# Optimization experiments

Hardware: AMD Instinct MI355X
Metric: run time of the kernel (lower is better)

Reference implementation:

```python
import jax, jax.numpy as jnp
import numpy as np

EMBED = 512
HEADS = 8
SCALE = 4
B, N = 2, 2048
DH = EMBED // HEADS
EPS = 1e-5


def _mha(q_in, k_in, v_in, wq, bq, wk, bk, wv, bv, wo, bo, causal):
    Bq, Nq, _ = q_in.shape
    Nk = k_in.shape[1]
    Q = (q_in @ wq + bq).reshape(Bq, Nq, HEADS, DH)
    K = (k_in @ wk + bk).reshape(Bq, Nk, HEADS, DH)
    V = (v_in @ wv + bv).reshape(Bq, Nk, HEADS, DH)
    # scores: [B, H, Nq, Nk]
    scores = jnp.einsum('bqhd,bkhd->bhqk', Q, K) / np.sqrt(DH).astype(np.float32)
    if causal:
        mask = jnp.triu(jnp.full((Nq, Nq), -jnp.inf, dtype=scores.dtype), k=1)
        scores = scores + mask[None, None]
    attn = jax.nn.softmax(scores, axis=-1)
    out = jnp.einsum('bhqk,bkhd->bqhd', attn, V).reshape(Bq, Nq, EMBED)
    return out @ wo + bo


def _ln(x, g, b):
    mu = jnp.mean(x, axis=-1, keepdims=True)
    var = jnp.var(x, axis=-1, keepdims=True)
    return (x - mu) * jax.lax.rsqrt(var + EPS) * g + b


def setup_inputs() -> dict:
    key = jax.random.key(0)
    ks = iter(jax.random.split(key, 32))
    p = lambda *s: 0.02 * jax.random.normal(next(ks), s, dtype=jnp.float32)
    inp = {
        'x': jax.random.normal(next(ks), (B, N, EMBED), dtype=jnp.float32),
        'encoder_output': jax.random.normal(next(ks), (B, N, EMBED), dtype=jnp.float32),
    }
    for pre in ('sa', 'ca'):
        inp[pre + '_wq'] = p(EMBED, EMBED); inp[pre + '_bq'] = jnp.zeros(EMBED)
        inp[pre + '_wk'] = p(EMBED, EMBED); inp[pre + '_bk'] = jnp.zeros(EMBED)
        inp[pre + '_wv'] = p(EMBED, EMBED); inp[pre + '_bv'] = jnp.zeros(EMBED)
        inp[pre + '_wo'] = p(EMBED, EMBED); inp[pre + '_bo'] = jnp.zeros(EMBED)
    for i in (1, 2, 3):
        inp[f'ln{i}_g'] = jnp.ones(EMBED); inp[f'ln{i}_b'] = jnp.zeros(EMBED)
    inp['ff_w1'] = p(EMBED, SCALE * EMBED); inp['ff_b1'] = jnp.zeros(SCALE * EMBED)
    inp['ff_w2'] = p(SCALE * EMBED, EMBED); inp['ff_b2'] = jnp.zeros(EMBED)
    return inp


def reference(x, encoder_output,
              sa_wq, sa_bq, sa_wk, sa_bk, sa_wv, sa_bv, sa_wo, sa_bo,
              ca_wq, ca_bq, ca_wk, ca_bk, ca_wv, ca_bv, ca_wo, ca_bo,
              ln1_g, ln1_b, ln2_g, ln2_b, ln3_g, ln3_b,
              ff_w1, ff_b1, ff_w2, ff_b2):
    x = _mha(x, x, x, sa_wq, sa_bq, sa_wk, sa_bk, sa_wv, sa_bv, sa_wo, sa_bo, True) + x
    x = _ln(x, ln1_g, ln1_b)
    x = _mha(x, encoder_output, encoder_output,
             ca_wq, ca_bq, ca_wk, ca_bk, ca_wv, ca_bv, ca_wo, ca_bo, False) + x
    x = _ln(x, ln2_g, ln2_b)
    h = jax.nn.gelu(x @ ff_w1 + ff_b1, approximate=False)
    x = h @ ff_w2 + ff_b2 + x
    return _ln(x, ln3_g, ln3_b)
```

## Files before the change

kernel.cpp:

```cpp
#include <hip/hip_runtime.h>
#include <hip/hip_bf16.h>

typedef __bf16 bf16x8 __attribute__((ext_vector_type(8)));
typedef float f32x4 __attribute__((ext_vector_type(4)));
typedef unsigned short u16;

#define EMB 512
#define FF 2048
#define MTOT 4096
#define SEQ 2048

__device__ __forceinline__ u16 f2b(float f) {
  return __builtin_bit_cast(u16, (__bf16)f);
}

__device__ __forceinline__ void gload16(const u16* g, u16* l) {
  __builtin_amdgcn_global_load_lds(
      (const __attribute__((address_space(1))) unsigned int*)g,
      (__attribute__((address_space(3))) unsigned int*)l, 16, 0, 0);
}

template <int N>
__device__ __forceinline__ void wait_vmcnt() {
  if constexpr (N == 0) asm volatile("s_waitcnt vmcnt(0)" ::: "memory");
  else if constexpr (N == 4) asm volatile("s_waitcnt vmcnt(4)" ::: "memory");
  else if constexpr (N == 6) asm volatile("s_waitcnt vmcnt(6)" ::: "memory");
  else if constexpr (N == 8) asm volatile("s_waitcnt vmcnt(8)" ::: "memory");
}

__global__ __launch_bounds__(256) void prep_all(
    const float* s0, const float* s1, const float* s2, const float* s3,
    const float* s4, const float* s5, const float* s6, const float* s7,
    const float* s8, const float* s9,
    u16* d0, u16* d1, u16* d2, u16* d3, u16* d4,
    u16* d5, u16* d6, u16* d7, u16* d8, u16* d9,
    const float* x, u16* xb, const float* enc, u16* encb,
    const float* bq1, const float* bk1, const float* bv1, float* bqkv,
    const float* bk2, const float* bv2, float* bkv) {
  int z = blockIdx.z, bx = blockIdx.x, by = blockIdx.y;
  int tid = threadIdx.x;
  if (z >= 10) {
    int fb = by * 64 + bx;
    const float* src = (z == 10) ? x : enc;
    u16* dst = (z == 10) ? xb : encb;
    size_t base = (size_t)fb * 2048 + tid * 8;
    float4 a = *(const float4*)(src + base);
    float4 b = *(const float4*)(src + base + 4);
    uint4 u;
    u.x = f2b(a.x) | ((unsigned)f2b(a.y) << 16);
    u.y = f2b(a.z) | ((unsigned)f2b(a.w) << 16);
    u.z = f2b(b.x) | ((unsigned)f2b(b.y) << 16);
    u.w = f2b(b.z) | ((unsigned)f2b(b.w) << 16);
    *(uint4*)(dst + base) = u;
    return;
  }
  if (z == 0 && bx == 16 && by == 0) {
    for (int i = tid; i < 1536; i += 256)
      bqkv[i] = (i < 512) ? bq1[i] : (i < 1024 ? bk1[i - 512] : bv1[i - 1024]);
    return;
  }
  if (z == 1 && bx == 16 && by == 0) {
    for (int i = tid; i < 1024; i += 256)
      bkv[i] = (i < 512) ? bk2[i] : bv2[i - 512];
    return;
  }
  const float* src; u16* dst; int K, N;
  switch (z) {
    case 0: src = s0; dst = d0; K = 512; N = 512; break;
    case 1: src = s1; dst = d1; K = 512; N = 512; break;
    case 2: src = s2; dst = d2; K = 512; N = 512; break;
    case 3: src = s3; dst = d3; K = 512; N = 512; break;
    case 4: src = s4; dst = d4; K = 512; N = 512; break;
    case 5: src = s5; dst = d5; K = 512; N = 512; break;
    case 6: src = s6; dst = d6; K = 512; N = 512; break;
    case 7: src = s7; dst = d7; K = 512; N = 512; break;
    case 8: src = s8; dst = d8; K = 512; N = 2048; break;
    default: src = s9; dst = d9; K = 2048; N = 512; break;
  }
  int ntl, ktl;
  if (z == 9) { ktl = bx; ntl = by; } else { ntl = bx; ktl = by; }
  if (ntl * 32 >= N || ktl * 32 >= K) return;
  __shared__ float t[32][33];
  int tx = tid & 31, ty = tid >> 5;
  int n0 = ntl * 32, k0 = ktl * 32;
#pragma unroll
  for (int i = 0; i < 4; i++)
    t[ty + i * 8][tx] = src[(size_t)(k0 + ty + i * 8) * N + n0 + tx];
  __syncthreads();
#pragma unroll
  for (int i = 0; i < 4; i++)
    dst[(size_t)(n0 + ty + i * 8) * K + k0 + tx] = f2b(t[tx][ty + i * 8]);
}

template <int BM, int BN, bool OUTB, bool OUTF, bool RES, bool GELU_>
__global__ __launch_bounds__(256) void gemm_bt(
    const u16* __restrict__ A, const u16* __restrict__ Bt,
    const float* __restrict__ bias, const float* __restrict__ resid,
    u16* __restrict__ outb, float* __restrict__ outf, int K, int Nd) {
  constexpr int MI = BM / 32;
  constexpr int NI = BN / 32;
  constexpr int RA = BM / 32;
  constexpr int RB = BN / 32;
  constexpr int L = RA + RB;
  __shared__ u16 As[2][BM * 64];
  __shared__ u16 Bs[2][BN * 64];
  int tid = threadIdx.x;
  int lane = tid & 63, w = tid >> 6;
  int g = lane >> 4, li = lane & 15;
  int wr = w >> 1, wc = w & 1;
  int m0 = blockIdx.x * BM, n0 = blockIdx.y * BN;
  int row_s = tid >> 3, ch_s = tid & 7;
  const u16* srcs[L];
  int ldsoff[L];
#pragma unroll
  for (int r = 0; r < L; r++) {
    int rr = (r < RA) ? r : r - RA;
    int row = rr * 32 + row_s;
    int csw = ch_s ^ (row & 7);
    srcs[r] = ((r < RA) ? A + (size_t)(m0 + row) * K : Bt + (size_t)(n0 + row) * K) + csw * 8;
    ldsoff[r] = (rr * 256 + tid) * 8;
  }
  f32x4 acc[MI][NI] = {};
  int T = K >> 6;
  auto stage = [&](int t, int buf) {
    int k0 = t << 6;
#pragma unroll
    for (int r = 0; r < RA; r++) gload16(srcs[r] + k0, &As[buf][ldsoff[r]]);
#pragma unroll
    for (int r = RA; r < L; r++) gload16(srcs[r] + k0, &Bs[buf][ldsoff[r]]);
  };
  stage(0, 0);
  stage(1, 1);
  for (int t = 0; t < T; t++) {
    int cur = t & 1;
    if (t == T - 1) wait_vmcnt<0>(); else wait_vmcnt<L>();
    __builtin_amdgcn_s_barrier();
    __builtin_amdgcn_sched_barrier(0);
    bf16x8 af[MI][2], bfr[NI][2];
#pragma unroll
    for (int i = 0; i < MI; i++) {
      int R = wr * (BM / 2) + i * 16 + li;
#pragma unroll
      for (int ks = 0; ks < 2; ks++)
        af[i][ks] = *(const bf16x8*)&As[cur][R * 64 + (((ks * 4 + g) ^ (R & 7)) * 8)];
    }
#pragma unroll
    for (int i = 0; i < NI; i++) {
      int R = wc * (BN / 2) + i * 16 + li;
#pragma unroll
      for (int ks = 0; ks < 2; ks++)
        bfr[i][ks] = *(const bf16x8*)&Bs[cur][R * 64 + (((ks * 4 + g) ^ (R & 7)) * 8)];
    }
#pragma unroll
    for (int mi = 0; mi < MI; mi++)
#pragma unroll
      for (int ni = 0; ni < NI; ni++)
#pragma unroll
        for (int ks = 0; ks < 2; ks++)
          acc[mi][ni] = __builtin_amdgcn_mfma_f32_16x16x32_bf16(af[mi][ks], bfr[ni][ks], acc[mi][ni], 0, 0, 0);
    __builtin_amdgcn_s_barrier();
    if (t + 2 < T) stage(t + 2, cur);
  }
#pragma unroll
  for (int mi = 0; mi < MI; mi++)
#pragma unroll
    for (int ni = 0; ni < NI; ni++) {
      int gn = n0 + wc * (BN / 2) + ni * 16 + li;
      float bv = bias[gn];
#pragma unroll
      for (int r = 0; r < 4; r++) {
        int gm = m0 + wr * (BM / 2) + mi * 16 + g * 4 + r;
        float v = acc[mi][ni][r] + bv;
        if (RES) v += resid[(size_t)gm * Nd + gn];
        if (GELU_) v = 0.5f * v * (1.0f + erff(v * 0.70710678118654752f));
        if (OUTF) outf[(size_t)gm * Nd + gn] = v;
        if (OUTB) outb[(size_t)gm * Nd + gn] = f2b(v);
      }
    }
}

template <bool CAUSAL>
__global__ __launch_bounds__(256) void attn_fwd(
    const u16* __restrict__ Q, const u16* __restrict__ Kp,
    const u16* __restrict__ Vp, u16* __restrict__ O, int qs, int kvs) {
  __shared__ u16 Ks[2][128 * 64];
  __shared__ u16 Vt[2][64 * 128];
  __shared__ u16 Ps[4][16 * 128];
  int tid = threadIdx.x;
  int lane = tid & 63, w = tid >> 6;
  int g = lane >> 4, li = lane & 15;
  int idx = blockIdx.x;
  int bh = idx & 15;
  int qbi = idx >> 4;
  if (CAUSAL) qbi = (SEQ / 64 - 1) - qbi;
  int qb = qbi * 64;
  int b = bh >> 3, h = bh & 7;
  const u16* Qh = Q + (size_t)b * SEQ * qs + h * 64;
  const u16* Kh = Kp + (size_t)b * SEQ * kvs + h * 64;
  const u16* Vh = Vp + (size_t)b * SEQ * kvs + h * 64;
  int qrow = qb + w * 16 + li;
  bf16x8 qa[2];
#pragma unroll
  for (int ks = 0; ks < 2; ks++) {
    bf16x8 tq = *(const bf16x8*)&Qh[(size_t)qrow * qs + ks * 32 + g * 8];
#pragma unroll
    for (int j = 0; j < 8; j++) tq[j] = (__bf16)((float)tq[j] * 0.18033688011112042f);
    qa[ks] = tq;
  }
  int kcc = lane & 7;
  const u16* Ksrc[4];
#pragma unroll
  for (int j = 0; j < 4; j++) {
    int row = j * 32 + w * 8 + (lane >> 3);
    int sw = ((j * 4 + w) ^ (lane >> 3)) & 7;
    Ksrc[j] = Kh + (size_t)row * kvs + (kcc ^ sw) * 8;
  }
  size_t kstep = (size_t)128 * kvs;
  int kq = tid & 31, dcv = tid >> 5;
  const u16* Vsrc = Vh + (size_t)(4 * kq) * kvs + dcv * 8;
  uint4 vr[4];
  auto stageK = [&](int t, int buf) {
    size_t o = (size_t)t * kstep;
    u16* dst = &Ks[buf][w * 512];
#pragma unroll
    for (int j = 0; j < 4; j++) gload16(Ksrc[j] + o, dst + j * 2048);
  };
  auto loadV = [&](int t) {
    size_t o = (size_t)t * kstep;
#pragma unroll
    for (int kk = 0; kk < 4; kk++)
      vr[kk] = *(const uint4*)(Vsrc + o + (size_t)kk * kvs);
  };
  auto writeV = [&](int buf) {
    const u16* a0 = (const u16*)&vr[0];
    const u16* a1 = (const u16*)&vr[1];
    const u16* a2 = (const u16*)&vr[2];
    const u16* a3 = (const u16*)&vr[3];
#pragma unroll
    for (int jj = 0; jj < 8; jj++) {
      int d = dcv * 8 + jj;
      int swv = ((d >> 3) ^ d) & 15;
      uint2 pk;
      pk.x = (unsigned)a0[jj] | ((unsigned)a1[jj] << 16);
      pk.y = (unsigned)a2[jj] | ((unsigned)a3[jj] << 16);
      *(uint2*)&Vt[buf][d * 128 + ((kq >> 1) ^ swv) * 8 + 4 * (kq & 1)] = pk;
    }
  };
  int T = CAUSAL ? (qb >> 7) + 1 : SEQ / 128;
  stageK(0, 0);
  loadV(0);
  writeV(0);
  __syncthreads();
  f32x4 o[4] = {};
  float mreg = -1e30f, lreg = 0.f;
  for (int t = 0; t < T; t++) {
    int cur = t & 1;
    if (t + 1 < T) { stageK(t + 1, cur ^ 1); loadV(t + 1); }
    int kv0 = t << 7;
    f32x4 S[8] = {};
    __builtin_amdgcn_s_setprio(1);
#pragma unroll
    for (int nt = 0; nt < 8; nt++) {
      int krow = nt * 16 + li;
      int sw = ((krow >> 3) ^ krow) & 7;
#pragma unroll
      for (int ks = 0; ks < 2; ks++) {
        bf16x8 kb = *(const bf16x8*)&Ks[cur][krow * 64 + ((ks * 4 + g) ^ sw) * 8];
        S[nt] = __builtin_amdgcn_mfma_f32_16x16x32_bf16(kb, qa[ks], S[nt], 0, 0, 0);
      }
    }
    __builtin_amdgcn_s_setprio(0);
    if (CAUSAL && (kv0 + 127 > qb + w * 16)) {
#pragma unroll
      for (int nt = 0; nt < 8; nt++) {
        int kb0 = kv0 + nt * 16 + g * 4;
#pragma unroll
        for (int r = 0; r < 4; r++)
          if (kb0 + r > qrow) S[nt][r] = -1e30f;
      }
    }
    f32x4 mx = S[0];
#pragma unroll
    for (int nt = 1; nt < 8; nt++)
#pragma unroll
      for (int r = 0; r < 4; r++) mx[r] = fmaxf(mx[r], S[nt][r]);
    float pm = fmaxf(fmaxf(mx[0], mx[1]), fmaxf(mx[2], mx[3]));
    pm = fmaxf(pm, __shfl_xor(pm, 16, 64));
    pm = fmaxf(pm, __shfl_xor(pm, 32, 64));
    bool need = __any(pm > mreg + 8.0f);
    float nm = need ? fmaxf(mreg, pm) : mreg;
    f32x4 acc4 = {0.f, 0.f, 0.f, 0.f};
#pragma unroll
    for (int nt = 0; nt < 8; nt++)
#pragma unroll
      for (int r = 0; r < 4; r++) {
        float e = exp2f(S[nt][r] - nm);
        S[nt][r] = e;
        acc4[r] += e;
      }
    float rs = (acc4[0] + acc4[1]) + (acc4[2] + acc4[3]);
    rs += __shfl_xor(rs, 16, 64);
    rs += __shfl_xor(rs, 32, 64);
    if (need) {
      float csc = exp2f(mreg - nm);
      lreg = lreg * csc + rs;
      mreg = nm;
      float cscr[4];
#pragma unroll
      for (int r = 0; r < 4; r++)
        cscr[r] = __shfl(csc, (lane & 48) | (g * 4 + r), 64);
#pragma unroll
      for (int nd = 0; nd < 4; nd++)
#pragma unroll
        for (int r = 0; r < 4; r++) o[nd][r] *= cscr[r];
    } else {
      lreg += rs;
    }
#pragma unroll
    for (int nt = 0; nt < 8; nt++) {
      int cp = 2 * nt + (g >> 1);
      uint2 pk;
      pk.x = (unsigned)f2b(S[nt][0]) | ((unsigned)f2b(S[nt][1]) << 16);
      pk.y = (unsigned)f2b(S[nt][2]) | ((unsigned)f2b(S[nt][3]) << 16);
      *(uint2*)&Ps[w][li * 128 + ((cp ^ li) * 8) + 4 * (g & 1)] = pk;
    }
    bf16x8 pa[4];
#pragma unroll
    for (int k2 = 0; k2 < 4; k2++)
      pa[k2] = *(const bf16x8*)&Ps[w][li * 128 + (((k2 * 4 + g) ^ li) * 8)];
    __builtin_amdgcn_s_setprio(1);
#pragma unroll
    for (int nd = 0; nd < 4; nd++) {
      int d = nd * 16 + li;
      int swv = ((d >> 3) ^ d) & 15;
#pragma unroll
      for (int k2 = 0; k2 < 4; k2++) {
        bf16x8 vb = *(const bf16x8*)&Vt[cur][d * 128 + (((k2 * 4 + g) ^ swv) * 8)];
        o[nd] = __builtin_amdgcn_mfma_f32_16x16x32_bf16(pa[k2], vb, o[nd], 0, 0, 0);
      }
    }
    __builtin_amdgcn_s_setprio(0);
    if (t + 1 < T) writeV(cur ^ 1);
    __syncthreads();
  }
  float linv = 1.0f / lreg;
  float invr[4];
#pragma unroll
  for (int r = 0; r < 4; r++)
    invr[r] = __shfl(linv, (lane & 48) | (g * 4 + r), 64);
#pragma unroll
  for (int nd = 0; nd < 4; nd++)
#pragma unroll
    for (int r = 0; r < 4; r++)
      O[(size_t)b * SEQ * EMB + (size_t)(qb + w * 16 + g * 4 + r) * EMB + h * 64 + nd * 16 + li] =
          f2b(o[nd][r] * invr[r]);
}

__global__ __launch_bounds__(256) void ln_fused(
    const float* __restrict__ in, const float* __restrict__ gamma,
    const float* __restrict__ beta, float* __restrict__ outf, u16* __restrict__ outb) {
  int row = blockIdx.x * 4 + (threadIdx.x >> 6);
  int lane = threadIdx.x & 63;
  const float* p = in + (size_t)row * EMB + lane * 8;
  float v[8];
  *(float4*)&v[0] = *(const float4*)p;
  *(float4*)&v[4] = *(const float4*)(p + 4);
  float s = 0.f, q = 0.f;
#pragma unroll
  for (int j = 0; j < 8; j++) { s += v[j]; q += v[j] * v[j]; }
#pragma unroll
  for (int d = 1; d < 64; d <<= 1) {
    s += __shfl_xor(s, d, 64);
    q += __shfl_xor(q, d, 64);
  }
  float mu = s * (1.0f / EMB);
  float var = q * (1.0f / EMB) - mu * mu;
  float rsig = rsqrtf(var + 1e-5f);
  float gg[8], bb[8];
  *(float4*)&gg[0] = *(const float4*)(gamma + lane * 8);
  *(float4*)&gg[4] = *(const float4*)(gamma + lane * 8 + 4);
  *(float4*)&bb[0] = *(const float4*)(beta + lane * 8);
  *(float4*)&bb[4] = *(const float4*)(beta + lane * 8 + 4);
  float o[8];
#pragma unroll
  for (int j = 0; j < 8; j++) o[j] = (v[j] - mu) * rsig * gg[j] + bb[j];
  float* po = outf + (size_t)row * EMB + lane * 8;
  *(float4*)po = *(float4*)&o[0];
  *(float4*)(po + 4) = *(float4*)&o[4];
  if (outb) {
    uint4 u;
    u.x = f2b(o[0]) | ((unsigned)f2b(o[1]) << 16);
    u.y = f2b(o[2]) | ((unsigned)f2b(o[3]) << 16);
    u.z = f2b(o[4]) | ((unsigned)f2b(o[5]) << 16);
    u.w = f2b(o[6]) | ((unsigned)f2b(o[7]) << 16);
    *(uint4*)(outb + (size_t)row * EMB + lane * 8) = u;
  }
}

extern "C" void kernel_launch(void* const* d_in, const int* in_sizes, int n_in,
                              void* d_out, int out_size, void* d_ws, size_t ws_size,
                              hipStream_t stream) {
  const float* x     = (const float*)d_in[0];
  const float* enc   = (const float*)d_in[1];
  const float* sa_wq = (const float*)d_in[2];
  const float* sa_bq = (const float*)d_in[3];
  const float* sa_wk = (const float*)d_in[4];
  const float* sa_bk = (const float*)d_in[5];
  const float* sa_wv = (const float*)d_in[6];
  const float* sa_bv = (const float*)d_in[7];
  const float* sa_wo = (const float*)d_in[8];
  const float* sa_bo = (const float*)d_in[9];
  const float* ca_wq = (const float*)d_in[10];
  const float* ca_bq = (const float*)d_in[11];
  const float* ca_wk = (const float*)d_in[12];
  const float* ca_bk = (const float*)d_in[13];
  const float* ca_wv = (const float*)d_in[14];
  const float* ca_bv = (const float*)d_in[15];
  const float* ca_wo = (const float*)d_in[16];
  const float* ca_bo = (const float*)d_in[17];
  const float* ln1_g = (const float*)d_in[18];
  const float* ln1_b = (const float*)d_in[19];
  const float* ln2_g = (const float*)d_in[20];
  const float* ln2_b = (const float*)d_in[21];
  const float* ln3_g = (const float*)d_in[22];
  const float* ln3_b = (const float*)d_in[23];
  const float* ff_w1 = (const float*)d_in[24];
  const float* ff_b1 = (const float*)d_in[25];
  const float* ff_w2 = (const float*)d_in[26];
  const float* ff_b2 = (const float*)d_in[27];

  char* ws = (char*)d_ws;
  size_t off = 0;
  auto alloc = [&](size_t bytes) {
    void* p = ws + off;
    off = (off + bytes + 255) & ~(size_t)255;
    return p;
  };
  u16* qkvT_sa  = (u16*)alloc((size_t)1536 * EMB * 2);
  u16* oT_sa    = (u16*)alloc((size_t)EMB * EMB * 2);
  u16* qT_ca    = (u16*)alloc((size_t)EMB * EMB * 2);
  u16* kvT_ca   = (u16*)alloc((size_t)1024 * EMB * 2);
  u16* oT_ca    = (u16*)alloc((size_t)EMB * EMB * 2);
  u16* w1T      = (u16*)alloc((size_t)FF * EMB * 2);
  u16* w2T      = (u16*)alloc((size_t)EMB * FF * 2);
  float* bqkv_sa = (float*)alloc(1536 * 4);
  float* bkv_ca  = (float*)alloc(1024 * 4);
  u16* xb    = (u16*)alloc((size_t)MTOT * EMB * 2);
  u16* encb  = (u16*)alloc((size_t)MTOT * EMB * 2);
  u16* qkv   = (u16*)alloc((size_t)MTOT * 1536 * 2);
  u16* attnb = (u16*)alloc((size_t)MTOT * EMB * 2);
  float* t0  = (float*)alloc((size_t)MTOT * EMB * 4);
  float* x1  = (float*)alloc((size_t)MTOT * EMB * 4);
  u16* x1b   = (u16*)alloc((size_t)MTOT * EMB * 2);
  float* x2  = (float*)alloc((size_t)MTOT * EMB * 4);
  u16* x2b   = (u16*)alloc((size_t)MTOT * EMB * 2);
  u16* hbuf  = (u16*)alloc((size_t)MTOT * FF * 2);
  u16* qca  = xb;
  u16* kvca = qkv;

  prep_all<<<dim3(64, 16, 12), 256, 0, stream>>>(
      sa_wq, sa_wk, sa_wv, sa_wo, ca_wq, ca_wk, ca_wv, ca_wo, ff_w1, ff_w2,
      qkvT_sa, qkvT_sa + 512 * EMB, qkvT_sa + 1024 * EMB, oT_sa, qT_ca,
      kvT_ca, kvT_ca + 512 * EMB, oT_ca, w1T, w2T,
      x, xb, enc, encb,
      sa_bq, sa_bk, sa_bv, bqkv_sa, ca_bk, ca_bv, bkv_ca);

  gemm_bt<128, 64, true, false, false, false><<<dim3(32, 24), 256, 0, stream>>>(
      xb, qkvT_sa, bqkv_sa, nullptr, qkv, nullptr, EMB, 1536);
  attn_fwd<true><<<512, 256, 0, stream>>>(qkv, qkv + 512, qkv + 1024, attnb, 1536, 1536);
  gemm_bt<64, 64, false, true, true, false><<<dim3(64, 8), 256, 0, stream>>>(
      attnb, oT_sa, sa_bo, x, nullptr, t0, EMB, EMB);
  ln_fused<<<1024, 256, 0, stream>>>(t0, ln1_g, ln1_b, x1, x1b);

  gemm_bt<64, 64, true, false, false, false><<<dim3(64, 8), 256, 0, stream>>>(
      x1b, qT_ca, ca_bq, nullptr, qca, nullptr, EMB, EMB);
  gemm_bt<128, 64, true, false, false, false><<<dim3(32, 16), 256, 0, stream>>>(
      encb, kvT_ca, bkv_ca, nullptr, kvca, nullptr, EMB, 1024);
  attn_fwd<false><<<512, 256, 0, stream>>>(qca, kvca, kvca + 512, attnb, EMB, 1024);
  gemm_bt<64, 64, false, true, true, false><<<dim3(64, 8), 256, 0, stream>>>(
      attnb, oT_ca, ca_bo, x1, nullptr, t0, EMB, EMB);
  ln_fused<<<1024, 256, 0, stream>>>(t0, ln2_g, ln2_b, x2, x2b);

  gemm_bt<128, 64, true, false, false, true><<<dim3(32, 32), 256, 0, stream>>>(
      x2b, w1T, ff_b1, nullptr, hbuf, nullptr, EMB, FF);
  gemm_bt<64, 64, false, true, true, false><<<dim3(64, 8), 256, 0, stream>>>(
      hbuf, w2T, ff_b2, x2, nullptr, t0, FF, EMB);
  ln_fused<<<1024, 256, 0, stream>>>(t0, ln3_g, ln3_b, (float*)d_out, nullptr);
}
```

Measured before the change: 325.7 us.

## Merge cross-attn Q and KV projections, enlarge GEMM tiles, rebalance causal order

Fuses the cross-attention Q projection (from x1) and KV projection (from encoder output) into one GEMM launch. Each block selects its A operand and output buffer by column range, which removes a kernel launch and its tail. Several projection GEMMs move from 128x64 to 128x128 tiles for more operand reuse, at the cost of fewer blocks and more registers per block. The causal attention block order changes so the second half of the grid runs short query blocks first, pairing heavy and light work across the grid.

After: 325.5 us. No clear change (-0.1%).

```diff
diff --git a/kernel.cpp b/kernel.cpp
--- a/kernel.cpp
+++ b/kernel.cpp
@@ -36,7 +36,7 @@
     u16* d5, u16* d6, u16* d7, u16* d8, u16* d9,
     const float* x, u16* xb, const float* enc, u16* encb,
     const float* bq1, const float* bk1, const float* bv1, float* bqkv,
-    const float* bk2, const float* bv2, float* bkv) {
+    const float* bq2, const float* bk2, const float* bv2, float* bca) {
   int z = blockIdx.z, bx = blockIdx.x, by = blockIdx.y;
   int tid = threadIdx.x;
   if (z >= 10) {
@@ -60,8 +60,8 @@
     return;
   }
   if (z == 1 && bx == 16 && by == 0) {
-    for (int i = tid; i < 1024; i += 256)
-      bkv[i] = (i < 512) ? bk2[i] : bv2[i - 512];
+    for (int i = tid; i < 1536; i += 256)
+      bca[i] = (i < 512) ? bq2[i] : (i < 1024 ? bk2[i - 512] : bv2[i - 1024]);
     return;
   }
   const float* src; u16* dst; int K, N;
@@ -92,11 +92,13 @@
     dst[(size_t)(n0 + ty + i * 8) * K + k0 + tx] = f2b(t[tx][ty + i * 8]);
 }
 
-template <int BM, int BN, bool OUTB, bool OUTF, bool RES, bool GELU_>
+template <int BM, int BN, bool OUTB, bool OUTF, bool RES, bool GELU_, bool SPLITN = false>
 __global__ __launch_bounds__(256) void gemm_bt(
-    const u16* __restrict__ A, const u16* __restrict__ Bt,
+    const u16* __restrict__ A, const u16* __restrict__ A2,
+    const u16* __restrict__ Bt,
     const float* __restrict__ bias, const float* __restrict__ resid,
-    u16* __restrict__ outb, float* __restrict__ outf, int K, int Nd) {
+    u16* __restrict__ outb, u16* __restrict__ outb2,
+    float* __restrict__ outf, int K, int Nd) {
   constexpr int MI = BM / 32;
   constexpr int NI = BN / 32;
   constexpr int RA = BM / 32;
@@ -109,6 +111,7 @@
   int g = lane >> 4, li = lane & 15;
   int wr = w >> 1, wc = w & 1;
   int m0 = blockIdx.x * BM, n0 = blockIdx.y * BN;
+  const u16* Abase = SPLITN ? (n0 < 512 ? A : A2) : A;
   int row_s = tid >> 3, ch_s = tid & 7;
   const u16* srcs[L];
   int ldsoff[L];
@@ -117,7 +120,7 @@
     int rr = (r < RA) ? r : r - RA;
     int row = rr * 32 + row_s;
     int csw = ch_s ^ (row & 7);
-    srcs[r] = ((r < RA) ? A + (size_t)(m0 + row) * K : Bt + (size_t)(n0 + row) * K) + csw * 8;
+    srcs[r] = ((r < RA) ? Abase + (size_t)(m0 + row) * K : Bt + (size_t)(n0 + row) * K) + csw * 8;
     ldsoff[r] = (rr * 256 + tid) * 8;
   }
   f32x4 acc[MI][NI] = {};
@@ -174,7 +177,12 @@
         if (RES) v += resid[(size_t)gm * Nd + gn];
         if (GELU_) v = 0.5f * v * (1.0f + erff(v * 0.70710678118654752f));
         if (OUTF) outf[(size_t)gm * Nd + gn] = v;
-        if (OUTB) outb[(size_t)gm * Nd + gn] = f2b(v);
+        if constexpr (SPLITN) {
+          if (gn < 512) outb[(size_t)gm * 512 + gn] = f2b(v);
+          else outb2[(size_t)gm * 1024 + gn - 512] = f2b(v);
+        } else if (OUTB) {
+          outb[(size_t)gm * Nd + gn] = f2b(v);
+        }
       }
     }
 }
@@ -192,7 +200,7 @@
   int idx = blockIdx.x;
   int bh = idx & 15;
   int qbi = idx >> 4;
-  if (CAUSAL) qbi = (SEQ / 64 - 1) - qbi;
+  if (CAUSAL) qbi = (idx < 256) ? (31 - qbi) : (qbi - 16);
   int qb = qbi * 64;
   int b = bh >> 3, h = bh & 7;
   const u16* Qh = Q + (size_t)b * SEQ * qs + h * 64;
@@ -438,13 +446,12 @@
   };
   u16* qkvT_sa  = (u16*)alloc((size_t)1536 * EMB * 2);
   u16* oT_sa    = (u16*)alloc((size_t)EMB * EMB * 2);
-  u16* qT_ca    = (u16*)alloc((size_t)EMB * EMB * 2);
-  u16* kvT_ca   = (u16*)alloc((size_t)1024 * EMB * 2);
+  u16* qkvT_ca  = (u16*)alloc((size_t)1536 * EMB * 2);
   u16* oT_ca    = (u16*)alloc((size_t)EMB * EMB * 2);
   u16* w1T      = (u16*)alloc((size_t)FF * EMB * 2);
   u16* w2T      = (u16*)alloc((size_t)EMB * FF * 2);
   float* bqkv_sa = (float*)alloc(1536 * 4);
-  float* bkv_ca  = (float*)alloc(1024 * 4);
+  float* bca     = (float*)alloc(1536 * 4);
   u16* xb    = (u16*)alloc((size_t)MTOT * EMB * 2);
   u16* encb  = (u16*)alloc((size_t)MTOT * EMB * 2);
   u16* qkv   = (u16*)alloc((size_t)MTOT * 1536 * 2);
@@ -460,30 +467,28 @@
 
   prep_all<<<dim3(64, 16, 12), 256, 0, stream>>>(
       sa_wq, sa_wk, sa_wv, sa_wo, ca_wq, ca_wk, ca_wv, ca_wo, ff_w1, ff_w2,
-      qkvT_sa, qkvT_sa + 512 * EMB, qkvT_sa + 1024 * EMB, oT_sa, qT_ca,
-      kvT_ca, kvT_ca + 512 * EMB, oT_ca, w1T, w2T,
+      qkvT_sa, qkvT_sa + 512 * EMB, qkvT_sa + 1024 * EMB, oT_sa, qkvT_ca,
+      qkvT_ca + 512 * EMB, qkvT_ca + 1024 * EMB, oT_ca, w1T, w2T,
       x, xb, enc, encb,
-      sa_bq, sa_bk, sa_bv, bqkv_sa, ca_bk, ca_bv, bkv_ca);
-
-  gemm_bt<128, 64, true, false, false, false><<<dim3(32, 24), 256, 0, stream>>>(
-      xb, qkvT_sa, bqkv_sa, nullptr, qkv, nullptr, EMB, 1536);
+      sa_bq, sa_bk, sa_bv, bqkv_sa, ca_bq, ca_bk, ca_bv, bca);
+
+  gemm_bt<128, 128, true, false, false, false><<<dim3(32, 12), 256, 0, stream>>>(
+      xb, nullptr, qkvT_sa, bqkv_sa, nullptr, qkv, nullptr, nullptr, EMB, 1536);
   attn_fwd<true><<<512, 256, 0, stream>>>(qkv, qkv + 512, qkv + 1024, attnb, 1536, 1536);
   gemm_bt<64, 64, false, true, true, false><<<dim3(64, 8), 256, 0, stream>>>(
-      attnb, oT_sa, sa_bo, x, nullptr, t0, EMB, EMB);
+      attnb, nullptr, oT_sa, sa_bo, x, nullptr, nullptr, t0, EMB, EMB);
   ln_fused<<<1024, 256, 0, stream>>>(t0, ln1_g, ln1_b, x1, x1b);
 
-  gemm_bt<64, 64, true, false, false, false><<<dim3(64, 8), 256, 0, stream>>>(
-      x1b, qT_ca, ca_bq, nullptr, qca, nullptr, EMB, EMB);
-  gemm_bt<128, 64, true, false, false, false><<<dim3(32, 16), 256, 0, stream>>>(
-      encb, kvT_ca, bkv_ca, nullptr, kvca, nullptr, EMB, 1024);
+  gemm_bt<128, 128, true, false, false, false, true><<<dim3(32, 12), 256, 0, stream>>>(
+      x1b, encb, qkvT_ca, bca, nullptr, qca, kvca, nullptr, EMB, 1536);
   attn_fwd<false><<<512, 256, 0, stream>>>(qca, kvca, kvca + 512, attnb, EMB, 1024);
   gemm_bt<64, 64, false, true, true, false><<<dim3(64, 8), 256, 0, stream>>>(
-      attnb, oT_ca, ca_bo, x1, nullptr, t0, EMB, EMB);
+      attnb, nullptr, oT_ca, ca_bo, x1, nullptr, nullptr, t0, EMB, EMB);
   ln_fused<<<1024, 256, 0, stream>>>(t0, ln2_g, ln2_b, x2, x2b);
 
-  gemm_bt<128, 64, true, false, false, true><<<dim3(32, 32), 256, 0, stream>>>(
-      x2b, w1T, ff_b1, nullptr, hbuf, nullptr, EMB, FF);
+  gemm_bt<128, 128, true, false, false, true><<<dim3(32, 16), 256, 0, stream>>>(
+      x2b, nullptr, w1T, ff_b1, nullptr, hbuf, nullptr, nullptr, EMB, FF);
   gemm_bt<64, 64, false, true, true, false><<<dim3(64, 8), 256, 0, stream>>>(
-      hbuf, w2T, ff_b2, x2, nullptr, t0, FF, EMB);
+      hbuf, nullptr, w2T, ff_b2, x2, nullptr, nullptr, t0, FF, EMB);
   ln_fused<<<1024, 256, 0, stream>>>(t0, ln3_g, ln3_b, (float*)d_out, nullptr);
 }
```
